# Optimization experiments

Measured on AMD Instinct MI355X. Metric: run time of the kernel, lower is better.

Reference implementation:

```python
import jax, jax.numpy as jnp
import numpy as np

B, C, H, W = 4, 512, 64, 64
INTER = 64  # C // channel_stride


def setup_inputs() -> dict:
    key = jax.random.key(0)
    ks = jax.random.split(key, 5)
    s = 0.02  # small init scale for numerical stability of softmax logits
    return {
        "inputs": jax.random.normal(ks[0], (B, C, H, W), dtype=jnp.float32),
        "Wq": jax.random.normal(ks[1], (INTER, C), dtype=jnp.float32) * s,
        "bq": jnp.zeros((INTER,), dtype=jnp.float32),
        "Wk": jax.random.normal(ks[2], (INTER, C), dtype=jnp.float32) * s,
        "bk": jnp.zeros((INTER,), dtype=jnp.float32),
        "Wv": jax.random.normal(ks[3], (C, C), dtype=jnp.float32) * s,
        "bv": jnp.zeros((C,), dtype=jnp.float32),
        "gamma": jax.random.normal(ks[4], (1,), dtype=jnp.float32),
    }


def reference(inputs, Wq, bq, Wk, bk, Wv, bv, gamma):
    b, c, h, w = inputs.shape
    n = h * w
    x = inputs.reshape(b, c, n)  # (B, C, N)
    # 1x1 convs == per-pixel linear projections
    q = jnp.einsum('dc,bcn->bnd', Wq, x) + bq            # (B, N, d)
    k = jnp.einsum('dc,bcn->bdn', Wk, x) + bk[:, None]   # (B, d, N)
    v = jnp.einsum('oc,bcn->bon', Wv, x) + bv[:, None]   # (B, O, N)
    # affinity: (B, Nq, Nk), softmax over keys (last dim), no scaling (as in source)
    affinity = jax.nn.softmax(jnp.einsum('bnd,bdm->bnm', q, k), axis=-1)
    # note: torch does bmm(value, affinity) -> out[b,o,m] = sum_j v[b,o,j] * A[b,j,m]
    out = jnp.einsum('bon,bnm->bom', v, affinity)        # (B, O, N)
    return gamma * out.reshape(b, -1, h, w) + inputs
```

## Files before the change

kernel.cpp:

```cpp
#include <hip/hip_runtime.h>
#include <stdint.h>

typedef __attribute__((ext_vector_type(8))) short short8;
typedef __attribute__((ext_vector_type(4))) float f32x4;
typedef __attribute__((ext_vector_type(8))) unsigned short u16x8;
typedef __attribute__((ext_vector_type(4))) unsigned short u16x4;
typedef __attribute__((ext_vector_type(2))) unsigned short u16x2;
typedef unsigned short u16;

#define NPIX 4096
#define CCH  512
#define DD   64


__device__ inline float b2f(u16 h){
  union { unsigned int i; float f; } u; u.i = ((unsigned int)h) << 16; return u.f;
}
__device__ inline u16 f2b(float f){
  union { float f; unsigned int i; } u; u.f = f;
  return (u16)((u.i + 0x7fffu + ((u.i >> 16) & 1u)) >> 16);
}
__device__ inline void gl2lds16(const void* g, void* l){
  __builtin_amdgcn_global_load_lds((const __attribute__((address_space(1))) unsigned int*)g,
                                   (__attribute__((address_space(3))) unsigned int*)l, 16, 0, 0);
}
__device__ inline f32x4 mfma16(short8 a, short8 b, f32x4 c){
  return __builtin_amdgcn_mfma_f32_16x16x32_bf16(a, b, c, 0, 0, 0);
}

__global__ __launch_bounds__(256) void k0_transpose(const float* __restrict__ x,
    u16* __restrict__ xT, const float* __restrict__ Wq, const float* __restrict__ Wk,
    const float* __restrict__ Wv, u16* __restrict__ Wqkb, u16* __restrict__ Wvb){
  if (blockIdx.z == 4){
    int bid = blockIdx.x * 8 + blockIdx.y;
    for (int r = 0; r < 3; ++r){
      int i = (r * 512 + bid) * 256 + threadIdx.x;
      if (i < 65536){
        int row = i >> 9, col = i & 511;
        float v = (row < 64) ? Wq[(row << 9) + col] : Wk[((row - 64) << 9) + col];
        Wqkb[(row << 9) + (col ^ ((row & 7) << 3))] = f2b(v);
      } else if (i < 327680){
        int j = i - 65536;
        int row = j >> 9, col = j & 511;
        Wvb[(row << 9) + (col ^ ((row & 7) << 3))] = f2b(Wv[j]);
      }
    }
    return;
  }
  __shared__ u16 tile[64][66];
  const int b = blockIdx.z;
  const int n0 = blockIdx.x * 64, c0 = blockIdx.y * 64;
  const float* xb = x + ((size_t)b * CCH + c0) * NPIX + n0;
  #pragma unroll
  for (int r = 0; r < 16; ++r){
    int id = r * 256 + threadIdx.x;
    int cc = id >> 6, nn = id & 63;
    tile[nn][cc] = f2b(xb[(size_t)cc * NPIX + nn]);
  }
  __syncthreads();
  u16* xTb = xT + ((size_t)b * NPIX + n0) * CCH + c0;
  #pragma unroll
  for (int r = 0; r < 8; ++r){
    int id = r * 256 + threadIdx.x;
    int nn = id >> 5, c2 = id & 31;
    int colp = (2 * c2) ^ ((nn & 7) << 3);
    *(u16x2*)(xTb + (size_t)nn * CCH + colp) = *(const u16x2*)&tile[nn][2 * c2];
  }
}

__global__ __launch_bounds__(256) void k1_qk(const u16* __restrict__ xT,
    const u16* __restrict__ Wqk, const float* __restrict__ bq,
    const float* __restrict__ bk, u16* __restrict__ Qb, u16* __restrict__ Kb){
  __shared__ __align__(16) u16 As[128*64];
  __shared__ __align__(16) u16 Bs[128*64];
  const int b  = blockIdx.z;
  const int n0 = blockIdx.x * 128;
  const u16* Ab = xT + ((size_t)b * NPIX + n0) * CCH;
  const int t = threadIdx.x, wave = t >> 6, lane = t & 63, q = lane >> 4, l16 = lane & 15;
  const int wr = (wave >> 1) * 64, wc = (wave & 1) * 64;
  const int sw = l16 & 7;
  f32x4 acc[4][4];
  #pragma unroll
  for (int i = 0; i < 4; ++i)
    #pragma unroll
    for (int j = 0; j < 4; ++j) acc[i][j] = (f32x4){0.f,0.f,0.f,0.f};

  for (int k0 = 0; k0 < CCH; k0 += 64){
    __syncthreads();
    #pragma unroll
    for (int r = 0; r < 4; ++r){
      int id = r * 256 + t;
      int row = id >> 3, ko = (id & 7) << 3;
      gl2lds16(Ab + (size_t)row * CCH + k0 + ko, &As[id * 8]);
      gl2lds16(Wqk + (size_t)row * CCH + k0 + ko, &Bs[id * 8]);
    }
    __syncthreads();
    #pragma unroll
    for (int s = 0; s < 2; ++s){
      const int ca = ((s*4 + q) ^ sw) << 3;
      short8 af[4], bfr[4];
      #pragma unroll
      for (int i = 0; i < 4; ++i){
        af[i]  = *(const short8*)&As[(wr + i*16 + l16)*64 + ca];
        bfr[i] = *(const short8*)&Bs[(wc + i*16 + l16)*64 + ca];
      }
      #pragma unroll
      for (int i = 0; i < 4; ++i)
        #pragma unroll
        for (int j = 0; j < 4; ++j)
          acc[i][j] = mfma16(af[i], bfr[j], acc[i][j]);
    }
  }
  #pragma unroll
  for (int i = 0; i < 4; ++i){
    #pragma unroll
    for (int j = 0; j < 4; ++j){
      int col = wc + j*16 + l16;
      #pragma unroll
      for (int r2 = 0; r2 < 4; ++r2){
        int n = n0 + wr + i*16 + q*4 + r2;
        int sw8 = (n & 7) << 3;
        float v = acc[i][j][r2];
        if (col < 64) Qb[((size_t)b * NPIX + n) * DD + (col ^ sw8)]        = f2b(v + bq[col]);
        else          Kb[((size_t)b * NPIX + n) * DD + ((col - 64) ^ sw8)] = f2b(v + bk[col - 64]);
      }
    }
  }
}

__global__ __launch_bounds__(256) void k2_v(const u16* __restrict__ xT,
    const u16* __restrict__ Wvb, const float* __restrict__ bv, u16* __restrict__ Vb){
  __shared__ __align__(16) u16 As[128*64];
  __shared__ __align__(16) u16 Bs[128*64];
  const int b  = blockIdx.z;
  const int n0 = blockIdx.x * 128;
  const int o0 = blockIdx.y * 128;
  const u16* Ab = Wvb + (size_t)o0 * CCH;
  const u16* Bb = xT + ((size_t)b * NPIX + n0) * CCH;
  const int t = threadIdx.x, wave = t >> 6, lane = t & 63, q = lane >> 4, l16 = lane & 15;
  const int wr = (wave >> 1) * 64, wc = (wave & 1) * 64;
  const int sw = l16 & 7;
  f32x4 acc[4][4];
  #pragma unroll
  for (int i = 0; i < 4; ++i)
    #pragma unroll
    for (int j = 0; j < 4; ++j) acc[i][j] = (f32x4){0.f,0.f,0.f,0.f};

  for (int k0 = 0; k0 < CCH; k0 += 64){
    __syncthreads();
    #pragma unroll
    for (int r = 0; r < 4; ++r){
      int id = r * 256 + t;
      int row = id >> 3, ko = (id & 7) << 3;
      gl2lds16(Ab + (size_t)row * CCH + k0 + ko, &As[id * 8]);
      gl2lds16(Bb + (size_t)row * CCH + k0 + ko, &Bs[id * 8]);
    }
    __syncthreads();
    #pragma unroll
    for (int s = 0; s < 2; ++s){
      const int ca = ((s*4 + q) ^ sw) << 3;
      short8 af[4], bfr[4];
      #pragma unroll
      for (int i = 0; i < 4; ++i){
        af[i]  = *(const short8*)&As[(wr + i*16 + l16)*64 + ca];
        bfr[i] = *(const short8*)&Bs[(wc + i*16 + l16)*64 + ca];
      }
      #pragma unroll
      for (int i = 0; i < 4; ++i)
        #pragma unroll
        for (int j = 0; j < 4; ++j)
          acc[i][j] = mfma16(af[i], bfr[j], acc[i][j]);
    }
  }
  #pragma unroll
  for (int i = 0; i < 4; ++i){
    #pragma unroll
    for (int j = 0; j < 4; ++j){
      int n = n0 + wc + j*16 + l16;
      #pragma unroll
      for (int r2 = 0; r2 < 4; ++r2){
        int o = o0 + wr + i*16 + q*4 + r2;
        int np = n ^ ((o & 7) << 3);
        Vb[((size_t)b * CCH + o) * NPIX + np] = f2b(acc[i][j][r2] + bv[o]);
      }
    }
  }
}

__global__ __launch_bounds__(256) void k3_logits(const u16* __restrict__ Qb,
    const u16* __restrict__ Kb, u16* __restrict__ E, float* __restrict__ Z, int b0){
  __shared__ __align__(16) u16 smem[128*136];
  u16* As = smem;
  u16* Bs = smem + 128*64;
  const int bloc = blockIdx.z, b = b0 + bloc;
  const int n0 = blockIdx.x * 128;
  const int m0 = blockIdx.y * 128;
  const u16* Ab = Kb + ((size_t)b * NPIX + m0) * DD;
  const u16* Bb = Qb + ((size_t)b * NPIX + n0) * DD;
  const int t = threadIdx.x, wave = t >> 6, lane = t & 63, q = lane >> 4, l16 = lane & 15;
  const int wr = (wave >> 1) * 64, wc = (wave & 1) * 64;
  const int sw = l16 & 7;
  f32x4 acc[4][4];
  #pragma unroll
  for (int i = 0; i < 4; ++i)
    #pragma unroll
    for (int j = 0; j < 4; ++j) acc[i][j] = (f32x4){0.f,0.f,0.f,0.f};

  #pragma unroll
  for (int r = 0; r < 4; ++r){
    int id = r * 256 + t;
    int row = id >> 3, ko = (id & 7) << 3;
    gl2lds16(Ab + row * DD + ko, &As[id * 8]);
    gl2lds16(Bb + row * DD + ko, &Bs[id * 8]);
  }
  __syncthreads();
  #pragma unroll
  for (int s = 0; s < 2; ++s){
    const int ca = ((s*4 + q) ^ sw) << 3;
    short8 af[4], bfr[4];
    #pragma unroll
    for (int i = 0; i < 4; ++i){
      af[i]  = *(const short8*)&As[(wr + i*16 + l16)*64 + ca];
      bfr[i] = *(const short8*)&Bs[(wc + i*16 + l16)*64 + ca];
    }
    #pragma unroll
    for (int i = 0; i < 4; ++i)
      #pragma unroll
      for (int j = 0; j < 4; ++j)
        acc[i][j] = mfma16(af[i], bfr[j], acc[i][j]);
  }
  __syncthreads();
  u16* tile = smem;
  float colsum[4] = {0.f, 0.f, 0.f, 0.f};
  #pragma unroll
  for (int i = 0; i < 4; ++i){
    #pragma unroll
    for (int j = 0; j < 4; ++j){
      #pragma unroll
      for (int r2 = 0; r2 < 4; ++r2){
        int mrow = wr + i*16 + q*4 + r2;
        int ncol = wc + j*16 + l16;
        float l = fminf(fmaxf(acc[i][j][r2], -60.f), 30.f);
        float e = __expf(l);
        tile[mrow * 136 + ncol] = f2b(e);
        colsum[j] += e;
      }
    }
  }
  #pragma unroll
  for (int j = 0; j < 4; ++j){
    float v = colsum[j];
    v += __shfl_xor(v, 16, 64);
    v += __shfl_xor(v, 32, 64);
    if (q == 0) atomicAdd(&Z[(size_t)b * NPIX + n0 + wc + j*16 + l16], v);
  }
  __syncthreads();
  u16* Eb = E + (size_t)bloc * NPIX * NPIX;
  #pragma unroll
  for (int r = 0; r < 8; ++r){
    int id = r * 256 + t;
    int row = id >> 4, chunk = id & 15;
    int g = chunk >> 3, c3 = chunk & 7;
    int colp = g * 64 + ((c3 ^ (row & 7)) << 3);
    *(u16x8*)(Eb + (size_t)(m0 + row) * NPIX + n0 + colp) =
        *(const u16x8*)&tile[row * 136 + chunk * 8];
  }
}

__global__ __launch_bounds__(256) void k3b_scale(u16* __restrict__ Vb,
    const float* __restrict__ Z, const float* __restrict__ gm, int b0){
  size_t i4  = ((size_t)blockIdx.x * 256 + threadIdx.x) * 4;
  size_t off = ((size_t)b0 << 21) + i4;
  int b = (int)(off >> 21);
  int o = (int)((off >> 12) & 511);
  int np = (int)(off & (NPIX - 1));
  int nl = np ^ ((o & 7) << 3);
  float g = gm[0];
  u16x4 vv = *(const u16x4*)(Vb + off);
  f32x4 zz = *(const f32x4*)(Z + ((size_t)b << 12) + nl);
  u16x4 r;
  #pragma unroll
  for (int k = 0; k < 4; ++k) r[k] = f2b(g * b2f(vv[k]) / fmaxf(zz[k], 1e-20f));
  *(u16x4*)(Vb + off) = r;
}

__global__ __launch_bounds__(256) void k4_out(const u16* __restrict__ Vs,
    const u16* __restrict__ E, const float* __restrict__ xin,
    float* __restrict__ outp, int b0){
  __shared__ __align__(16) u16 As[128*128];
  __shared__ __align__(16) u16 Bs[128*128];
  const int bloc = blockIdx.z, b = b0 + bloc;
  const int m0 = blockIdx.x * 128;
  const int o0 = blockIdx.y * 128;
  const u16* Ab = Vs + ((size_t)b * CCH + o0) * NPIX;
  const u16* Bb = E + (size_t)bloc * NPIX * NPIX + (size_t)m0 * NPIX;
  const int t = threadIdx.x, wave = t >> 6, lane = t & 63, q = lane >> 4, l16 = lane & 15;
  const int wr = (wave >> 1) * 64, wc = (wave & 1) * 64;
  const int sw = l16 & 7;
  f32x4 acc[4][4];
  #pragma unroll
  for (int i = 0; i < 4; ++i)
    #pragma unroll
    for (int j = 0; j < 4; ++j) acc[i][j] = (f32x4){0.f,0.f,0.f,0.f};

  for (int k0 = 0; k0 < NPIX; k0 += 128){
    __syncthreads();
    #pragma unroll
    for (int r = 0; r < 8; ++r){
      int id = r * 256 + t;
      int row = id >> 4, ko = (id & 15) << 3;
      gl2lds16(Ab + (size_t)row * NPIX + k0 + ko, &As[id * 8]);
      gl2lds16(Bb + (size_t)row * NPIX + k0 + ko, &Bs[id * 8]);
    }
    __syncthreads();
    #pragma unroll
    for (int s = 0; s < 4; ++s){
      const int ca = ((s >> 1) << 6) + (((((s & 1) << 2) + q) ^ sw) << 3);
      short8 af[4], bfr[4];
      #pragma unroll
      for (int i = 0; i < 4; ++i){
        af[i]  = *(const short8*)&As[(wr + i*16 + l16)*128 + ca];
        bfr[i] = *(const short8*)&Bs[(wc + i*16 + l16)*128 + ca];
      }
      #pragma unroll
      for (int i = 0; i < 4; ++i)
        #pragma unroll
        for (int j = 0; j < 4; ++j)
          acc[i][j] = mfma16(af[i], bfr[j], acc[i][j]);
    }
  }
  const float* xb = xin + (size_t)b * CCH * NPIX;
  float* ob = outp + (size_t)b * CCH * NPIX;
  #pragma unroll
  for (int i = 0; i < 4; ++i){
    #pragma unroll
    for (int j = 0; j < 4; ++j){
      int m = m0 + wc + j*16 + l16;
      #pragma unroll
      for (int r2 = 0; r2 < 4; ++r2){
        int o = o0 + wr + i*16 + q*4 + r2;
        size_t idx = (size_t)o * NPIX + m;
        ob[idx] = acc[i][j][r2] + xb[idx];
      }
    }
  }
}

extern "C" void kernel_launch(void* const* d_in, const int* in_sizes, int n_in,
                              void* d_out, int out_size, void* d_ws, size_t ws_size,
                              hipStream_t stream){
  (void)in_sizes; (void)n_in; (void)out_size;
  const float* x  = (const float*)d_in[0];
  const float* Wq = (const float*)d_in[1];
  const float* bq = (const float*)d_in[2];
  const float* Wk = (const float*)d_in[3];
  const float* bk = (const float*)d_in[4];
  const float* Wv = (const float*)d_in[5];
  const float* bv = (const float*)d_in[6];
  const float* gm = (const float*)d_in[7];
  float* outp = (float*)d_out;

  char* ws = (char*)d_ws;
  u16*  Qb   = (u16*)(ws + 0);
  u16*  Kb   = (u16*)(ws + 2097152);
  u16*  Vb   = (u16*)(ws + 4194304);
  float* Z   = (float*)(ws + 20971520);
  u16*  Wqkb = (u16*)(ws + 21037056);
  u16*  Wvb  = (u16*)(ws + 21168128);
  u16*  xT   = (u16*)(ws + 21692416);
  u16*  E    = (u16*)(ws + 21692416);

  const size_t ebytes = (size_t)NPIX * NPIX * 2;
  const size_t base   = 21692416;
  if (ws_size < base + ebytes){
    return;
  }
  int NB = 1;
  if (ws_size >= base + 4 * ebytes) NB = 4;
  else if (ws_size >= base + 2 * ebytes) NB = 2;

  hipMemsetAsync(Z, 0, (size_t)4 * NPIX * sizeof(float), stream);
  k0_transpose<<<dim3(64, 8, 5), 256, 0, stream>>>(x, xT, Wq, Wk, Wv, Wqkb, Wvb);
  k1_qk<<<dim3(32, 1, 4), 256, 0, stream>>>(xT, Wqkb, bq, bk, Qb, Kb);
  k2_v<<<dim3(32, 4, 4), 256, 0, stream>>>(xT, Wvb, bv, Vb);
  for (int b0 = 0; b0 < 4; b0 += NB){
    int nb = NB; if (b0 + nb > 4) nb = 4 - b0;
    k3_logits<<<dim3(32, 32, nb), 256, 0, stream>>>(Qb, Kb, E, Z, b0);
    k3b_scale<<<dim3(nb * 2048), 256, 0, stream>>>(Vb, Z, gm, b0);
    k4_out<<<dim3(32, 4, nb), 256, 0, stream>>>(Vb, E, x, outp, b0);
  }
}
```

Measured before the change: 227.6 us.

## Pipeline k4_out with triple-buffered LDS and larger 128x256 tiles

Rewrites the output GEMM kernel to use 512-thread blocks computing 128x256 tiles with a K-step of 64. A three-stage LDS ring is filled by async global-to-LDS loads issued two iterations ahead, with explicit waitcnt, barriers and raised MFMA priority. The aim is to hide global-load latency behind MFMA work and cut E re-reads by widening the tile. In exchange it uses more LDS per block, relies on hand-tuned vmcnt accounting and may lower occupancy.

```diff
diff --git a/kernel.cpp b/kernel.cpp
--- a/kernel.cpp
+++ b/kernel.cpp
@@ -284,61 +284,109 @@
   *(u16x4*)(Vb + off) = r;
 }
 
-__global__ __launch_bounds__(256) void k4_out(const u16* __restrict__ Vs,
+__global__ __launch_bounds__(512, 2) void k4_out(const u16* __restrict__ Vs,
     const u16* __restrict__ E, const float* __restrict__ xin,
     float* __restrict__ outp, int b0){
-  __shared__ __align__(16) u16 As[128*128];
-  __shared__ __align__(16) u16 Bs[128*128];
+  __shared__ __align__(16) u16 As[3][128*64];
+  __shared__ __align__(16) u16 Bs[3][256*64];
   const int bloc = blockIdx.z, b = b0 + bloc;
-  const int m0 = blockIdx.x * 128;
+  const int m0 = blockIdx.x * 256;
   const int o0 = blockIdx.y * 128;
   const u16* Ab = Vs + ((size_t)b * CCH + o0) * NPIX;
   const u16* Bb = E + (size_t)bloc * NPIX * NPIX + (size_t)m0 * NPIX;
   const int t = threadIdx.x, wave = t >> 6, lane = t & 63, q = lane >> 4, l16 = lane & 15;
-  const int wr = (wave >> 1) * 64, wc = (wave & 1) * 64;
+  const int ar = (wave >> 2) * 64;
+  const int br = (wave & 3) * 64;
   const int sw = l16 & 7;
+
+  auto stageA = [&](int kt, int bi){
+    const int k0 = kt << 6;
+    #pragma unroll
+    for (int r = 0; r < 2; ++r){
+      int id = r * 512 + t;
+      gl2lds16(Ab + (size_t)(id >> 3) * NPIX + (k0 + ((id & 7) << 3)), &As[bi][id * 8]);
+    }
+  };
+  auto stageBh = [&](int kt, int bi, int half){
+    const int k0 = kt << 6;
+    #pragma unroll
+    for (int r = 0; r < 2; ++r){
+      int id = (half * 2 + r) * 512 + t;
+      gl2lds16(Bb + (size_t)(id >> 3) * NPIX + (k0 + ((id & 7) << 3)), &Bs[bi][id * 8]);
+    }
+  };
+
   f32x4 acc[4][4];
   #pragma unroll
   for (int i = 0; i < 4; ++i)
     #pragma unroll
     for (int j = 0; j < 4; ++j) acc[i][j] = (f32x4){0.f,0.f,0.f,0.f};
 
-  for (int k0 = 0; k0 < NPIX; k0 += 128){
-    __syncthreads();
-    #pragma unroll
-    for (int r = 0; r < 8; ++r){
-      int id = r * 256 + t;
-      int row = id >> 4, ko = (id & 15) << 3;
-      gl2lds16(Ab + (size_t)row * NPIX + k0 + ko, &As[id * 8]);
-      gl2lds16(Bb + (size_t)row * NPIX + k0 + ko, &Bs[id * 8]);
-    }
-    __syncthreads();
-    #pragma unroll
-    for (int s = 0; s < 4; ++s){
-      const int ca = ((s >> 1) << 6) + (((((s & 1) << 2) + q) ^ sw) << 3);
-      short8 af[4], bfr[4];
-      #pragma unroll
-      for (int i = 0; i < 4; ++i){
-        af[i]  = *(const short8*)&As[(wr + i*16 + l16)*128 + ca];
-        bfr[i] = *(const short8*)&Bs[(wc + i*16 + l16)*128 + ca];
-      }
+  stageA(0, 0); stageBh(0, 0, 0); stageBh(0, 0, 1);
+  stageA(1, 1); stageBh(1, 1, 0); stageBh(1, 1, 1);
+  asm volatile("s_waitcnt vmcnt(6)" ::: "memory");
+  __builtin_amdgcn_sched_barrier(0);
+  __builtin_amdgcn_s_barrier();
+
+  int bi = 0;
+  for (int kt = 0; kt < NPIX / 64; ++kt){
+    const int bi2 = (bi >= 1) ? bi - 1 : bi + 2;
+    const bool pf = (kt + 2) < NPIX / 64;
+    short8 af[4], bfr[4];
+    {
+      const int ca = (q ^ sw) << 3;
+      #pragma unroll
+      for (int i = 0; i < 4; ++i) af[i]  = *(const short8*)&As[bi][(ar + i*16 + l16)*64 + ca];
+      #pragma unroll
+      for (int j = 0; j < 4; ++j) bfr[j] = *(const short8*)&Bs[bi][(br + j*16 + l16)*64 + ca];
+      if (pf){ stageA(kt + 2, bi2); stageBh(kt + 2, bi2, 0); }
+      __builtin_amdgcn_s_barrier();
+      asm volatile("s_waitcnt lgkmcnt(0)" ::: "memory");
+      __builtin_amdgcn_sched_barrier(0);
+      __builtin_amdgcn_s_setprio(1);
       #pragma unroll
       for (int i = 0; i < 4; ++i)
         #pragma unroll
         for (int j = 0; j < 4; ++j)
           acc[i][j] = mfma16(af[i], bfr[j], acc[i][j]);
-    }
-  }
+      __builtin_amdgcn_s_setprio(0);
+      __builtin_amdgcn_s_barrier();
+    }
+    {
+      const int ca = ((4 + q) ^ sw) << 3;
+      #pragma unroll
+      for (int i = 0; i < 4; ++i) af[i]  = *(const short8*)&As[bi][(ar + i*16 + l16)*64 + ca];
+      #pragma unroll
+      for (int j = 0; j < 4; ++j) bfr[j] = *(const short8*)&Bs[bi][(br + j*16 + l16)*64 + ca];
+      if (pf) stageBh(kt + 2, bi2, 1);
+      __builtin_amdgcn_s_barrier();
+      asm volatile("s_waitcnt lgkmcnt(0)" ::: "memory");
+      __builtin_amdgcn_sched_barrier(0);
+      __builtin_amdgcn_s_setprio(1);
+      #pragma unroll
+      for (int i = 0; i < 4; ++i)
+        #pragma unroll
+        for (int j = 0; j < 4; ++j)
+          acc[i][j] = mfma16(af[i], bfr[j], acc[i][j]);
+      __builtin_amdgcn_s_setprio(0);
+      if (kt < NPIX / 64 - 2){ asm volatile("s_waitcnt vmcnt(6)" ::: "memory"); }
+      else                   { asm volatile("s_waitcnt vmcnt(0)" ::: "memory"); }
+      __builtin_amdgcn_sched_barrier(0);
+      __builtin_amdgcn_s_barrier();
+    }
+    bi = (bi == 2) ? 0 : bi + 1;
+  }
+
   const float* xb = xin + (size_t)b * CCH * NPIX;
   float* ob = outp + (size_t)b * CCH * NPIX;
   #pragma unroll
   for (int i = 0; i < 4; ++i){
     #pragma unroll
     for (int j = 0; j < 4; ++j){
-      int m = m0 + wc + j*16 + l16;
+      int m = m0 + br + j*16 + l16;
       #pragma unroll
       for (int r2 = 0; r2 < 4; ++r2){
-        int o = o0 + wr + i*16 + q*4 + r2;
+        int o = o0 + ar + i*16 + q*4 + r2;
         size_t idx = (size_t)o * NPIX + m;
         ob[idx] = acc[i][j][r2] + xb[idx];
       }
@@ -387,6 +435,6 @@
     int nb = NB; if (b0 + nb > 4) nb = 4 - b0;
     k3_logits<<<dim3(32, 32, nb), 256, 0, stream>>>(Qb, Kb, E, Z, b0);
     k3b_scale<<<dim3(nb * 2048), 256, 0, stream>>>(Vb, Z, gm, b0);
-    k4_out<<<dim3(32, 4, nb), 256, 0, stream>>>(Vb, E, x, outp, b0);
-  }
-}
+    k4_out<<<dim3(16, 4, nb), 512, 0, stream>>>(Vb, E, x, outp, b0);
+  }
+}
```

Result: slower. 243.2 us (+6.8%).
